# Kernel optimization log

Measured on AMD Instinct MI355X. Metric: run time of the kernel, lower is better.

The kernel has to match this reference:

```python
import jax, jax.numpy as jnp
import numpy as np

BN_EPS = 1e-5
RES_SCALE = 0.7


def setup_inputs() -> dict:
    key = jax.random.key(0)
    ks = jax.random.split(key, 10)
    N, IN_DIM, HID, E, L = 50000, 2000, 64, 1600000, 4
    features = jax.random.normal(ks[0], (N, IN_DIM), dtype=jnp.float32)
    edges = jax.random.randint(ks[1], (2, E), 0, N, dtype=jnp.int64)
    # GCNConv params: layer 0 is in_dim->hid, layers 1..3 are hid->hid
    W0 = jax.random.normal(ks[2], (IN_DIM, HID), dtype=jnp.float32) / np.sqrt(IN_DIM)
    b0 = jnp.zeros((HID,), dtype=jnp.float32)
    Wh = jax.random.normal(ks[3], (L - 1, HID, HID), dtype=jnp.float32) / np.sqrt(HID)
    bh = jnp.zeros((L - 1, HID), dtype=jnp.float32)
    # BatchNorm1d affine params per layer
    gamma = jnp.ones((L, HID), dtype=jnp.float32)
    beta = jnp.zeros((L, HID), dtype=jnp.float32)
    # learned layer-mixing weights (torch.randn init)
    lw = jax.random.normal(ks[4], (L,), dtype=jnp.float32)
    return {"features": features, "edges": edges, "W0": W0, "b0": b0,
            "Wh": Wh, "bh": bh, "gamma": gamma, "beta": beta, "lw": lw}


def reference(features, edges, W0, b0, Wh, bh, gamma, beta, lw):
    n = features.shape[0]
    src, dst = edges[0], edges[1]
    # GCN symmetric normalization with self-loops, edge_weight=1
    deg = jnp.zeros((n,), features.dtype).at[dst].add(1.0) + 1.0  # +1 self loop
    dinv = jax.lax.rsqrt(deg)
    enorm = dinv[src] * dinv[dst]       # [E]
    snorm = dinv * dinv                 # [N], self-loop norm

    def gcn_conv(x, W, b):
        xw = x @ W                                            # [N, H]
        agg = jnp.zeros_like(xw).at[dst].add(xw[src] * enorm[:, None])
        agg = agg + xw * snorm[:, None]
        return agg + b

    def batchnorm(x, g, bt):
        m = x.mean(axis=0)
        v = x.var(axis=0)  # biased variance, as in BN training normalization
        return (x - m) * jax.lax.rsqrt(v + BN_EPS) * g + bt

    L = gamma.shape[0]
    Ws = [W0] + [Wh[i] for i in range(L - 1)]
    bs = [b0] + [bh[i] for i in range(L - 1)]

    layer_out = []
    x = features
    for i in range(L):
        x = gcn_conv(x, Ws[i], bs[i])
        x = jax.nn.relu(batchnorm(x, gamma[i], beta[i]))
        if i > 0:
            x = x + RES_SCALE * layer_out[i - 1]
        layer_out.append(x)

    w = jax.nn.softmax(lw)
    emb = layer_out[0] * w[0]
    for i in range(1, L):
        emb = emb + layer_out[i] * w[i]
    return emb
```

## Files before the change

kernel.cpp:

```cpp
#include <hip/hip_runtime.h>
#include <hip/hip_bf16.h>
#include <math.h>

#define BN_EPS 1e-5f
#define RES_SCALE 0.7f

typedef float f4 __attribute__((ext_vector_type(4)));
typedef short s8 __attribute__((ext_vector_type(8)));

__device__ inline short f2bf(float f) {
    __hip_bfloat16 h = __float2bfloat16(f);
    return *reinterpret_cast<short*>(&h);
}

__global__ __launch_bounds__(256) void k_zero(int* counts, int* cursor, float* stats, int N, int S) {
    int i = blockIdx.x * 256 + threadIdx.x;
    if (i < N) { counts[i] = 0; cursor[i] = 0; }
    if (i < S) stats[i] = 0.0f;
}

__global__ __launch_bounds__(256) void k_count(const int* __restrict__ edges, int E, int* __restrict__ counts) {
    int e = blockIdx.x * 256 + threadIdx.x;
    if (e < E) atomicAdd(&counts[edges[E + e]], 1);
}

__global__ __launch_bounds__(256) void k_scan1(const int* __restrict__ counts, int* __restrict__ bsum,
                                               float* __restrict__ dinv, int N) {
    __shared__ int sd[256];
    int t = threadIdx.x;
    int base = blockIdx.x * 1024 + t * 4;
    int s = 0;
    if (base + 3 < N) {
        int4 v = *(const int4*)(counts + base);
        s = v.x + v.y + v.z + v.w;
        f4 d;
        d.x = rsqrtf((float)v.x + 1.0f);
        d.y = rsqrtf((float)v.y + 1.0f);
        d.z = rsqrtf((float)v.z + 1.0f);
        d.w = rsqrtf((float)v.w + 1.0f);
        *(f4*)(dinv + base) = d;
    } else {
        for (int j = 0; j < 4; ++j) if (base + j < N) {
            int cv = counts[base + j];
            s += cv;
            dinv[base + j] = rsqrtf((float)cv + 1.0f);
        }
    }
    sd[t] = s; __syncthreads();
    for (int off = 128; off > 0; off >>= 1) { if (t < off) sd[t] += sd[t + off]; __syncthreads(); }
    if (t == 0) bsum[blockIdx.x] = sd[0];
}

__global__ void k_scan2(int* bsum, int B, int* rowstart, int N) {
    if (threadIdx.x == 0 && blockIdx.x == 0) {
        int run = 0;
        for (int b = 0; b < B; ++b) { int v = bsum[b]; bsum[b] = run; run += v; }
        rowstart[N] = run;
    }
}

__global__ __launch_bounds__(256) void k_scan3(const int* __restrict__ counts, const int* __restrict__ bsum,
                                               int* __restrict__ rowstart, int N) {
    __shared__ int sd[256];
    int t = threadIdx.x;
    int base = blockIdx.x * 1024 + t * 4;
    int v0 = 0, v1 = 0, v2 = 0, v3 = 0;
    if (base + 3 < N) { int4 v = *(const int4*)(counts + base); v0 = v.x; v1 = v.y; v2 = v.z; v3 = v.w; }
    else {
        if (base < N) v0 = counts[base];
        if (base + 1 < N) v1 = counts[base + 1];
        if (base + 2 < N) v2 = counts[base + 2];
        if (base + 3 < N) v3 = counts[base + 3];
    }
    int s = v0 + v1 + v2 + v3;
    sd[t] = s; __syncthreads();
    for (int off = 1; off < 256; off <<= 1) {
        int add = (t >= off) ? sd[t - off] : 0;
        __syncthreads();
        sd[t] += add;
        __syncthreads();
    }
    int excl = sd[t] - s + bsum[blockIdx.x];
    if (base < N)     rowstart[base]     = excl;
    if (base + 1 < N) rowstart[base + 1] = excl + v0;
    if (base + 2 < N) rowstart[base + 2] = excl + v0 + v1;
    if (base + 3 < N) rowstart[base + 3] = excl + v0 + v1 + v2;
}

__global__ __launch_bounds__(256) void k_scatter(const int* __restrict__ edges, int E,
                                                 const int* __restrict__ rowstart, int* __restrict__ cursor,
                                                 int* __restrict__ colA) {
    int e = blockIdx.x * 256 + threadIdx.x;
    if (e >= E) return;
    int s = edges[e], d = edges[E + e];
    int pos = rowstart[d] + atomicAdd(&cursor[d], 1);
    colA[pos] = s;
}

__global__ __launch_bounds__(256) void k_wt(const float* __restrict__ W0, const float* __restrict__ Wh,
                                            short* __restrict__ WT0, short* __restrict__ WTh, int K0) {
    __shared__ short Ts[64][72];
    int b = blockIdx.x, t = threadIdx.x;
    int nk0 = (K0 + 63) >> 6;
    const float* W; short* dst; int K, kt;
    if (b < nk0) { W = W0; dst = WT0; K = K0; kt = b * 64; }
    else { int l = b - nk0; W = Wh + (size_t)l * 64 * 64; dst = WTh + (size_t)l * 64 * 64; K = 64; kt = 0; }
    #pragma unroll
    for (int i = 0; i < 16; ++i) {
        int idx = t + i * 256;
        int r = idx >> 6, c = idx & 63;
        int gk = kt + r;
        Ts[c][r] = (gk < K) ? f2bf(W[(size_t)gk * 64 + c]) : (short)0;
    }
    __syncthreads();
    #pragma unroll
    for (int i = 0; i < 16; ++i) {
        int idx = t + i * 256;
        int n = idx >> 6, r = idx & 63;
        int gk = kt + r;
        if (gk < K) dst[(size_t)n * K + gk] = Ts[n][r];
    }
}

__global__ __launch_bounds__(256) void k_mm(const float* __restrict__ X, const short* __restrict__ WT,
                                            const float* __restrict__ dinv,
                                            __hip_bfloat16* __restrict__ Cb, int N, int K) {
    __shared__ float Xs[64][68];
    __shared__ short Ws[64][72];
    int t = threadIdx.x;
    int w = t >> 6, lane = t & 63;
    int m = lane & 15, kq = lane >> 4;
    int row0 = blockIdx.x * 64;

    int xr = t >> 3, xc = t & 7;
    int wn = t >> 2, wc = t & 3;

    f4 acc[4] = {};
    f4 px0, px1, px2, px3; int4 pw0, pw1;

    {
        int gr0 = row0 + xr, gr1 = row0 + xr + 32;
        int gk0 = xc * 4, gk1 = 32 + xc * 4;
        px0 = (gr0 < N && gk0 < K) ? *(const f4*)(X + (size_t)gr0 * K + gk0) : (f4){};
        px1 = (gr0 < N && gk1 < K) ? *(const f4*)(X + (size_t)gr0 * K + gk1) : (f4){};
        px2 = (gr1 < N && gk0 < K) ? *(const f4*)(X + (size_t)gr1 * K + gk0) : (f4){};
        px3 = (gr1 < N && gk1 < K) ? *(const f4*)(X + (size_t)gr1 * K + gk1) : (f4){};
        int gw0 = wc * 8, gw1 = 32 + wc * 8;
        pw0 = (gw0 < K) ? *(const int4*)(WT + (size_t)wn * K + gw0) : make_int4(0, 0, 0, 0);
        pw1 = (gw1 < K) ? *(const int4*)(WT + (size_t)wn * K + gw1) : make_int4(0, 0, 0, 0);
    }

    for (int kt = 0; kt < K; kt += 64) {
        *(f4*)&Xs[xr][xc * 4]           = px0;
        *(f4*)&Xs[xr][32 + xc * 4]      = px1;
        *(f4*)&Xs[xr + 32][xc * 4]      = px2;
        *(f4*)&Xs[xr + 32][32 + xc * 4] = px3;
        *(int4*)&Ws[wn][wc * 8]         = pw0;
        *(int4*)&Ws[wn][32 + wc * 8]    = pw1;
        __syncthreads();

        int kn = kt + 64;
        if (kn < K) {
            int gr0 = row0 + xr, gr1 = row0 + xr + 32;
            int gk0 = kn + xc * 4, gk1 = kn + 32 + xc * 4;
            px0 = (gr0 < N && gk0 < K) ? *(const f4*)(X + (size_t)gr0 * K + gk0) : (f4){};
            px1 = (gr0 < N && gk1 < K) ? *(const f4*)(X + (size_t)gr0 * K + gk1) : (f4){};
            px2 = (gr1 < N && gk0 < K) ? *(const f4*)(X + (size_t)gr1 * K + gk0) : (f4){};
            px3 = (gr1 < N && gk1 < K) ? *(const f4*)(X + (size_t)gr1 * K + gk1) : (f4){};
            int gw0 = kn + wc * 8, gw1 = kn + 32 + wc * 8;
            pw0 = (gw0 < K) ? *(const int4*)(WT + (size_t)wn * K + gw0) : make_int4(0, 0, 0, 0);
            pw1 = (gw1 < K) ? *(const int4*)(WT + (size_t)wn * K + gw1) : make_int4(0, 0, 0, 0);
        }

        int arow = w * 16 + m;
        f4 a00 = *(const f4*)&Xs[arow][kq * 8];
        f4 a01 = *(const f4*)&Xs[arow][kq * 8 + 4];
        f4 a10 = *(const f4*)&Xs[arow][32 + kq * 8];
        f4 a11 = *(const f4*)&Xs[arow][32 + kq * 8 + 4];
        s8 av0, av1;
        #pragma unroll
        for (int j = 0; j < 4; ++j) {
            av0[j] = f2bf(a00[j]); av0[j + 4] = f2bf(a01[j]);
            av1[j] = f2bf(a10[j]); av1[j + 4] = f2bf(a11[j]);
        }
        #pragma unroll
        for (int ct = 0; ct < 4; ++ct) {
            s8 bv0 = *(const s8*)&Ws[ct * 16 + m][kq * 8];
            s8 bv1 = *(const s8*)&Ws[ct * 16 + m][32 + kq * 8];
            acc[ct] = __builtin_amdgcn_mfma_f32_16x16x32_bf16(av0, bv0, acc[ct], 0, 0, 0);
            acc[ct] = __builtin_amdgcn_mfma_f32_16x16x32_bf16(av1, bv1, acc[ct], 0, 0, 0);
        }
        __syncthreads();
    }

    #pragma unroll
    for (int reg = 0; reg < 4; ++reg) {
        int gr = row0 + w * 16 + kq * 4 + reg;
        if (gr < N) {
            float di = dinv[gr];
            #pragma unroll
            for (int ct = 0; ct < 4; ++ct)
                Cb[(size_t)gr * 64 + ct * 16 + m] = __float2bfloat16(acc[ct][reg] * di);
        }
    }
}

__device__ inline const unsigned* g_rowsel(const unsigned* xw32, int c, int p, bool lo32) {
    unsigned o0 = (unsigned)__builtin_amdgcn_readlane(c, 2 * p) << 5;
    unsigned o1 = (unsigned)__builtin_amdgcn_readlane(c, 2 * p + 1) << 5;
    return xw32 + (lo32 ? o0 : o1);
}

__global__ __launch_bounds__(256) void k_gather(const __hip_bfloat16* __restrict__ xw, const int* __restrict__ colA,
                                                const int* __restrict__ rowstart,
                                                const float* __restrict__ dinv, float* __restrict__ agg, int N) {
    int wave = (blockIdx.x * 256 + threadIdx.x) >> 6;
    int lane = threadIdx.x & 63;
    if (wave >= N) return;
    int r = wave;
    const unsigned* xw32 = (const unsigned*)xw;
    int l31 = lane & 31;
    bool lo32 = lane < 32;

    unsigned vs = xw32[((size_t)(unsigned)r << 5) | l31];
    float acc0 = lo32 ? __uint_as_float(vs << 16) : 0.0f;
    float acc1 = lo32 ? __uint_as_float(vs & 0xffff0000u) : 0.0f;

    int b = rowstart[r], e = rowstart[r + 1];
    for (int base = b; base < e; base += 64) {
        int idx = base + lane;
        int c = (idx < e) ? colA[idx] : 0;
        int cnt = min(64, e - base);
        int npair = cnt >> 1;
        int j = 0;
        for (; j + 3 < npair; j += 4) {
            unsigned v0 = g_rowsel(xw32, c, j,     lo32)[l31];
            unsigned v1 = g_rowsel(xw32, c, j + 1, lo32)[l31];
            unsigned v2 = g_rowsel(xw32, c, j + 2, lo32)[l31];
            unsigned v3 = g_rowsel(xw32, c, j + 3, lo32)[l31];
            acc0 += __uint_as_float(v0 << 16); acc1 += __uint_as_float(v0 & 0xffff0000u);
            acc0 += __uint_as_float(v1 << 16); acc1 += __uint_as_float(v1 & 0xffff0000u);
            acc0 += __uint_as_float(v2 << 16); acc1 += __uint_as_float(v2 & 0xffff0000u);
            acc0 += __uint_as_float(v3 << 16); acc1 += __uint_as_float(v3 & 0xffff0000u);
        }
        for (; j < npair; ++j) {
            unsigned v = g_rowsel(xw32, c, j, lo32)[l31];
            acc0 += __uint_as_float(v << 16); acc1 += __uint_as_float(v & 0xffff0000u);
        }
        if (cnt & 1) {
            int s = __builtin_amdgcn_readlane(c, cnt - 1);
            unsigned v = xw32[((size_t)(unsigned)s << 5) | l31];
            if (lo32) {
                acc0 += __uint_as_float(v << 16);
                acc1 += __uint_as_float(v & 0xffff0000u);
            }
        }
    }
    acc0 += __shfl_xor(acc0, 32);
    acc1 += __shfl_xor(acc1, 32);
    if (lo32) {
        float di = dinv[r];
        float2 o; o.x = acc0 * di; o.y = acc1 * di;
        *(float2*)(agg + ((size_t)r << 6) + l31 * 2) = o;
    }
}

__global__ __launch_bounds__(256) void k_stats(const float* __restrict__ x, float* __restrict__ stats, int N) {
    int col = threadIdx.x & 63;
    int sub = threadIdx.x >> 6;
    float s = 0.f, s2 = 0.f;
    for (int r = blockIdx.x * 4 + sub; r < N; r += gridDim.x * 4) {
        float v = x[(size_t)r * 64 + col];
        s += v; s2 += v * v;
    }
    __shared__ float sd[2][4][64];
    sd[0][sub][col] = s; sd[1][sub][col] = s2;
    __syncthreads();
    if (sub == 0) {
        s  = sd[0][0][col] + sd[0][1][col] + sd[0][2][col] + sd[0][3][col];
        s2 = sd[1][0][col] + sd[1][1][col] + sd[1][2][col] + sd[1][3][col];
        atomicAdd(&stats[col], s);
        atomicAdd(&stats[64 + col], s2);
    }
}

__global__ __launch_bounds__(256) void k_elem(const float* __restrict__ agg, const float* __restrict__ stats,
                                              const float* __restrict__ gamma, const float* __restrict__ beta,
                                              const float* __restrict__ lw, const float* __restrict__ xprev,
                                              float* __restrict__ xcur, float* __restrict__ emb,
                                              int N, int layer, int L) {
    size_t i = ((size_t)blockIdx.x * 256 + threadIdx.x) * 4;
    if (i >= (size_t)N * 64) return;
    int c = (int)(i & 63);
    float rN = 1.0f / (float)N;
    f4 av = *(const f4*)(agg + i);
    f4 gv = *(const f4*)(gamma + c);
    f4 bv = *(const f4*)(beta + c);
    f4 sv = *(const f4*)(stats + c);
    f4 qv = *(const f4*)(stats + 64 + c);
    f4 v;
    #pragma unroll
    for (int j = 0; j < 4; ++j) {
        float mn = sv[j] * rN;
        float var = qv[j] * rN - mn * mn;
        float inv = rsqrtf(var + BN_EPS);
        v[j] = fmaxf((av[j] - mn) * inv * gv[j] + bv[j], 0.0f);
    }
    f4 xp = {};
    if (layer > 0) {
        xp = *(const f4*)(xprev + i);
        #pragma unroll
        for (int j = 0; j < 4; ++j) v[j] += RES_SCALE * xp[j];
    }
    if (layer < L - 1) *(f4*)(xcur + i) = v;
    if (layer == 0) return;

    float mx = lw[0];
    for (int j = 1; j < L; ++j) mx = fmaxf(mx, lw[j]);
    float sum = 0.f, wbuf[8];
    for (int j = 0; j < L; ++j) { float ee = __expf(lw[j] - mx); wbuf[j] = ee; sum += ee; }
    float rs = 1.0f / sum;
    float wl = wbuf[layer] * rs;
    f4 o;
    if (layer == 1) {
        float w0 = wbuf[0] * rs;
        #pragma unroll
        for (int j = 0; j < 4; ++j) o[j] = w0 * xp[j] + wl * v[j];
    } else {
        f4 ep = *(const f4*)(emb + i);
        #pragma unroll
        for (int j = 0; j < 4; ++j) o[j] = ep[j] + wl * v[j];
    }
    *(f4*)(emb + i) = o;
}

extern "C" void kernel_launch(void* const* d_in, const int* in_sizes, int n_in,
                              void* d_out, int out_size, void* d_ws, size_t ws_size,
                              hipStream_t stream) {
    const float* features = (const float*)d_in[0];
    const int*   edges    = (const int*)d_in[1];
    const float* W0       = (const float*)d_in[2];
    const float* Wh       = (const float*)d_in[4];
    const float* gamma    = (const float*)d_in[6];
    const float* beta     = (const float*)d_in[7];
    const float* lw       = (const float*)d_in[8];

    const int HID    = in_sizes[3];
    const int IN_DIM = in_sizes[2] / HID;
    const int N      = in_sizes[0] / IN_DIM;
    const int E      = in_sizes[1] / 2;
    const int L      = in_sizes[8];
    float* out = (float*)d_out;

    char* ws = (char*)d_ws;
    auto alloc = [&](size_t bytes) { char* p = ws; ws += (bytes + 255) & ~(size_t)255; return p; };
    int*   counts   = (int*)alloc((size_t)N * 4);
    int*   cursor   = (int*)alloc((size_t)N * 4);
    int*   rowstart = (int*)alloc((size_t)(N + 1) * 4);
    int*   bsum     = (int*)alloc(256 * 4);
    float* dinv     = (float*)alloc((size_t)N * 4);
    float* stats    = (float*)alloc((size_t)L * 128 * 4);
    int*   colA     = (int*)alloc((size_t)E * 4);
    short* WT0      = (short*)alloc((size_t)HID * IN_DIM * 2);
    short* WTh      = (short*)alloc((size_t)(L - 1) * HID * HID * 2);
    __hip_bfloat16* xw = (__hip_bfloat16*)alloc((size_t)N * HID * 2);
    float* agg      = (float*)alloc((size_t)N * HID * 4);
    float* x0       = (float*)alloc((size_t)N * HID * 4);
    float* x1       = (float*)alloc((size_t)N * HID * 4);

    int S = L * 128;
    int zgrid = (max(N, S) + 255) / 256;
    k_zero<<<zgrid, 256, 0, stream>>>(counts, cursor, stats, N, S);

    int egrid = (E + 255) / 256;
    k_count<<<egrid, 256, 0, stream>>>(edges, E, counts);

    int B = (N + 1023) / 1024;
    k_scan1<<<B, 256, 0, stream>>>(counts, bsum, dinv, N);
    k_scan2<<<1, 64, 0, stream>>>(bsum, B, rowstart, N);
    k_scan3<<<B, 256, 0, stream>>>(counts, bsum, rowstart, N);
    k_scatter<<<egrid, 256, 0, stream>>>(edges, E, rowstart, cursor, colA);

    int nk0 = (IN_DIM + 63) / 64;
    k_wt<<<nk0 + (L - 1), 256, 0, stream>>>(W0, Wh, WT0, WTh, IN_DIM);

    int mmgrid = (N + 63) / 64;
    int ggrid  = (N + 3) / 4;
    int elgrid = (int)(((size_t)N * HID / 4 + 255) / 256);

    float* xb[2] = { x0, x1 };
    const float* xc_prev = nullptr;
    for (int l = 0; l < L; ++l) {
        const float* Xin = (l == 0) ? features : xc_prev;
        int K = (l == 0) ? IN_DIM : HID;
        const short* WTl = (l == 0) ? WT0 : WTh + (size_t)(l - 1) * HID * HID;
        k_mm<<<mmgrid, 256, 0, stream>>>(Xin, WTl, dinv, xw, N, K);
        k_gather<<<ggrid, 256, 0, stream>>>(xw, colA, rowstart, dinv, agg, N);
        k_stats<<<256, 256, 0, stream>>>(agg, stats + l * 128, N);
        float* xcur = (l < L - 1) ? xb[l & 1] : nullptr;
        const float* xprev = (l == 0) ? nullptr : xb[(l - 1) & 1];
        k_elem<<<elgrid, 256, 0, stream>>>(agg, stats + l * 128, gamma + l * HID, beta + l * HID,
                                           lw, xprev, xcur, out, N, l, L);
        if (l < L - 1) xc_prev = xcur;
    }
}
```

Measured before the change: 1.006 ms.

## Fuse BN/residual elementwise with next-layer 64x64 matmul; double-buffer prefetch in k_mm

```diff
diff --git a/kernel.cpp b/kernel.cpp
--- a/kernel.cpp
+++ b/kernel.cpp
@@ -7,6 +7,7 @@
 
 typedef float f4 __attribute__((ext_vector_type(4)));
 typedef short s8 __attribute__((ext_vector_type(8)));
+typedef short bs4 __attribute__((ext_vector_type(4)));
 
 __device__ inline short f2bf(float f) {
     __hip_bfloat16 h = __float2bfloat16(f);
@@ -122,6 +123,50 @@
     }
 }
 
+#define MM_ISSUE(PX0, PX1, PX2, PX3, PW0, PW1, KT)                                        \
+    {                                                                                      \
+        int gr0_ = row0 + xr, gr1_ = gr0_ + 32;                                            \
+        int gk0_ = (KT) + xc * 4, gk1_ = (KT) + 32 + xc * 4;                               \
+        PX0 = (gr0_ < N && gk0_ < K) ? *(const f4*)(X + (size_t)gr0_ * K + gk0_) : (f4){}; \
+        PX1 = (gr0_ < N && gk1_ < K) ? *(const f4*)(X + (size_t)gr0_ * K + gk1_) : (f4){}; \
+        PX2 = (gr1_ < N && gk0_ < K) ? *(const f4*)(X + (size_t)gr1_ * K + gk0_) : (f4){}; \
+        PX3 = (gr1_ < N && gk1_ < K) ? *(const f4*)(X + (size_t)gr1_ * K + gk1_) : (f4){}; \
+        int gw0_ = (KT) + wc * 8, gw1_ = (KT) + 32 + wc * 8;                               \
+        PW0 = (gw0_ < K) ? *(const int4*)(WT + (size_t)wn * K + gw0_) : make_int4(0,0,0,0);\
+        PW1 = (gw1_ < K) ? *(const int4*)(WT + (size_t)wn * K + gw1_) : make_int4(0,0,0,0);\
+    }
+
+#define MM_BODY(PX0, PX1, PX2, PX3, PW0, PW1, KT)                                          \
+    {                                                                                      \
+        *(f4*)&Xs[xr][xc * 4]           = PX0;                                             \
+        *(f4*)&Xs[xr][32 + xc * 4]      = PX1;                                             \
+        *(f4*)&Xs[xr + 32][xc * 4]      = PX2;                                             \
+        *(f4*)&Xs[xr + 32][32 + xc * 4] = PX3;                                             \
+        *(int4*)&Ws[wn][wc * 8]         = PW0;                                             \
+        *(int4*)&Ws[wn][32 + wc * 8]    = PW1;                                             \
+        if ((KT) + 128 < K) MM_ISSUE(PX0, PX1, PX2, PX3, PW0, PW1, (KT) + 128);            \
+        __syncthreads();                                                                   \
+        int arow_ = w * 16 + m;                                                            \
+        f4 a00 = *(const f4*)&Xs[arow_][kq * 8];                                           \
+        f4 a01 = *(const f4*)&Xs[arow_][kq * 8 + 4];                                       \
+        f4 a10 = *(const f4*)&Xs[arow_][32 + kq * 8];                                      \
+        f4 a11 = *(const f4*)&Xs[arow_][32 + kq * 8 + 4];                                  \
+        s8 av0, av1;                                                                       \
+        _Pragma("unroll")                                                                  \
+        for (int j = 0; j < 4; ++j) {                                                      \
+            av0[j] = f2bf(a00[j]); av0[j + 4] = f2bf(a01[j]);                              \
+            av1[j] = f2bf(a10[j]); av1[j + 4] = f2bf(a11[j]);                              \
+        }                                                                                  \
+        _Pragma("unroll")                                                                  \
+        for (int ct = 0; ct < 4; ++ct) {                                                   \
+            s8 bv0 = *(const s8*)&Ws[ct * 16 + m][kq * 8];                                 \
+            s8 bv1 = *(const s8*)&Ws[ct * 16 + m][32 + kq * 8];                            \
+            acc[ct] = __builtin_amdgcn_mfma_f32_16x16x32_bf16(av0, bv0, acc[ct], 0, 0, 0); \
+            acc[ct] = __builtin_amdgcn_mfma_f32_16x16x32_bf16(av1, bv1, acc[ct], 0, 0, 0); \
+        }                                                                                  \
+        __syncthreads();                                                                   \
+    }
+
 __global__ __launch_bounds__(256) void k_mm(const float* __restrict__ X, const short* __restrict__ WT,
                                             const float* __restrict__ dinv,
                                             __hip_bfloat16* __restrict__ Cb, int N, int K) {
@@ -136,61 +181,15 @@
     int wn = t >> 2, wc = t & 3;
 
     f4 acc[4] = {};
-    f4 px0, px1, px2, px3; int4 pw0, pw1;
-
-    {
-        int gr0 = row0 + xr, gr1 = row0 + xr + 32;
-        int gk0 = xc * 4, gk1 = 32 + xc * 4;
-        px0 = (gr0 < N && gk0 < K) ? *(const f4*)(X + (size_t)gr0 * K + gk0) : (f4){};
-        px1 = (gr0 < N && gk1 < K) ? *(const f4*)(X + (size_t)gr0 * K + gk1) : (f4){};
-        px2 = (gr1 < N && gk0 < K) ? *(const f4*)(X + (size_t)gr1 * K + gk0) : (f4){};
-        px3 = (gr1 < N && gk1 < K) ? *(const f4*)(X + (size_t)gr1 * K + gk1) : (f4){};
-        int gw0 = wc * 8, gw1 = 32 + wc * 8;
-        pw0 = (gw0 < K) ? *(const int4*)(WT + (size_t)wn * K + gw0) : make_int4(0, 0, 0, 0);
-        pw1 = (gw1 < K) ? *(const int4*)(WT + (size_t)wn * K + gw1) : make_int4(0, 0, 0, 0);
-    }
-
-    for (int kt = 0; kt < K; kt += 64) {
-        *(f4*)&Xs[xr][xc * 4]           = px0;
-        *(f4*)&Xs[xr][32 + xc * 4]      = px1;
-        *(f4*)&Xs[xr + 32][xc * 4]      = px2;
-        *(f4*)&Xs[xr + 32][32 + xc * 4] = px3;
-        *(int4*)&Ws[wn][wc * 8]         = pw0;
-        *(int4*)&Ws[wn][32 + wc * 8]    = pw1;
-        __syncthreads();
-
-        int kn = kt + 64;
-        if (kn < K) {
-            int gr0 = row0 + xr, gr1 = row0 + xr + 32;
-            int gk0 = kn + xc * 4, gk1 = kn + 32 + xc * 4;
-            px0 = (gr0 < N && gk0 < K) ? *(const f4*)(X + (size_t)gr0 * K + gk0) : (f4){};
-            px1 = (gr0 < N && gk1 < K) ? *(const f4*)(X + (size_t)gr0 * K + gk1) : (f4){};
-            px2 = (gr1 < N && gk0 < K) ? *(const f4*)(X + (size_t)gr1 * K + gk0) : (f4){};
-            px3 = (gr1 < N && gk1 < K) ? *(const f4*)(X + (size_t)gr1 * K + gk1) : (f4){};
-            int gw0 = kn + wc * 8, gw1 = kn + 32 + wc * 8;
-            pw0 = (gw0 < K) ? *(const int4*)(WT + (size_t)wn * K + gw0) : make_int4(0, 0, 0, 0);
-            pw1 = (gw1 < K) ? *(const int4*)(WT + (size_t)wn * K + gw1) : make_int4(0, 0, 0, 0);
-        }
-
-        int arow = w * 16 + m;
-        f4 a00 = *(const f4*)&Xs[arow][kq * 8];
-        f4 a01 = *(const f4*)&Xs[arow][kq * 8 + 4];
-        f4 a10 = *(const f4*)&Xs[arow][32 + kq * 8];
-        f4 a11 = *(const f4*)&Xs[arow][32 + kq * 8 + 4];
-        s8 av0, av1;
-        #pragma unroll
-        for (int j = 0; j < 4; ++j) {
-            av0[j] = f2bf(a00[j]); av0[j + 4] = f2bf(a01[j]);
-            av1[j] = f2bf(a10[j]); av1[j + 4] = f2bf(a11[j]);
-        }
-        #pragma unroll
-        for (int ct = 0; ct < 4; ++ct) {
-            s8 bv0 = *(const s8*)&Ws[ct * 16 + m][kq * 8];
-            s8 bv1 = *(const s8*)&Ws[ct * 16 + m][32 + kq * 8];
-            acc[ct] = __builtin_amdgcn_mfma_f32_16x16x32_bf16(av0, bv0, acc[ct], 0, 0, 0);
-            acc[ct] = __builtin_amdgcn_mfma_f32_16x16x32_bf16(av1, bv1, acc[ct], 0, 0, 0);
-        }
-        __syncthreads();
+    f4 pxA0, pxA1, pxA2, pxA3; int4 pwA0, pwA1;
+    f4 pxB0, pxB1, pxB2, pxB3; int4 pwB0, pwB1;
+
+    MM_ISSUE(pxA0, pxA1, pxA2, pxA3, pwA0, pwA1, 0);
+    if (64 < K) MM_ISSUE(pxB0, pxB1, pxB2, pxB3, pwB0, pwB1, 64);
+
+    for (int kt = 0; kt < K; kt += 128) {
+        MM_BODY(pxA0, pxA1, pxA2, pxA3, pwA0, pwA1, kt);
+        if (kt + 64 < K) MM_BODY(pxB0, pxB1, pxB2, pxB3, pwB0, pwB1, kt + 64);
     }
 
     #pragma unroll
@@ -284,6 +283,105 @@
     }
 }
 
+__global__ __launch_bounds__(256) void k_elemmm(const float* __restrict__ agg, const float* __restrict__ stats,
+                                                const float* __restrict__ gamma, const float* __restrict__ beta,
+                                                const float* __restrict__ lw, const float* __restrict__ xprev,
+                                                float* __restrict__ xcur, float* __restrict__ emb,
+                                                const short* __restrict__ WT, const float* __restrict__ dinv,
+                                                __hip_bfloat16* __restrict__ xw,
+                                                int N, int layer, int L) {
+    __shared__ short Xb[64][72];
+    __shared__ short Ws[64][72];
+    int t = threadIdx.x;
+    int row0 = blockIdx.x * 64;
+
+    {
+        int n = t >> 3, c8 = (t & 7) * 8;
+        *(int4*)&Ws[n][c8]      = *(const int4*)(WT + n * 64 + c8);
+        *(int4*)&Ws[n + 32][c8] = *(const int4*)(WT + (n + 32) * 64 + c8);
+    }
+
+    int r = t >> 2, q = t & 3;
+    int gr = row0 + r;
+    bool valid = gr < N;
+    float rN = 1.0f / (float)N;
+    size_t base = (size_t)gr * 64 + q * 16;
+
+    float mx = lw[0];
+    for (int j = 1; j < L; ++j) mx = fmaxf(mx, lw[j]);
+    float sum = 0.f, wbuf[8];
+    for (int j = 0; j < L; ++j) { float ee = __expf(lw[j] - mx); wbuf[j] = ee; sum += ee; }
+    float rs = 1.0f / sum;
+    float wl = wbuf[layer] * rs, w0 = wbuf[0] * rs;
+
+    #pragma unroll
+    for (int j = 0; j < 4; ++j) {
+        int c = q * 16 + j * 4;
+        f4 av = valid ? *(const f4*)(agg + base + j * 4) : (f4){};
+        f4 sv = *(const f4*)(stats + c);
+        f4 qv = *(const f4*)(stats + 64 + c);
+        f4 gv = *(const f4*)(gamma + c);
+        f4 bv = *(const f4*)(beta + c);
+        f4 v;
+        #pragma unroll
+        for (int jj = 0; jj < 4; ++jj) {
+            float mn = sv[jj] * rN;
+            float var = qv[jj] * rN - mn * mn;
+            float inv = rsqrtf(var + BN_EPS);
+            v[jj] = fmaxf((av[jj] - mn) * inv * gv[jj] + bv[jj], 0.0f);
+        }
+        f4 xp = {};
+        if (layer > 0) {
+            if (valid) xp = *(const f4*)(xprev + base + j * 4);
+            #pragma unroll
+            for (int jj = 0; jj < 4; ++jj) v[jj] += RES_SCALE * xp[jj];
+        }
+        if (valid) *(f4*)(xcur + base + j * 4) = v;
+        if (layer >= 1 && valid) {
+            f4 o;
+            if (layer == 1) {
+                #pragma unroll
+                for (int jj = 0; jj < 4; ++jj) o[jj] = w0 * xp[jj] + wl * v[jj];
+            } else {
+                f4 ep = *(const f4*)(emb + base + j * 4);
+                #pragma unroll
+                for (int jj = 0; jj < 4; ++jj) o[jj] = ep[jj] + wl * v[jj];
+            }
+            *(f4*)(emb + base + j * 4) = o;
+        }
+        bs4 xb;
+        #pragma unroll
+        for (int jj = 0; jj < 4; ++jj) xb[jj] = f2bf(v[jj]);
+        *(bs4*)&Xb[r][q * 16 + j * 4] = xb;
+    }
+    __syncthreads();
+
+    int w = t >> 6, lane = t & 63;
+    int m = lane & 15, kq = lane >> 4;
+    f4 acc[4] = {};
+    int arow = w * 16 + m;
+    s8 av0 = *(const s8*)&Xb[arow][kq * 8];
+    s8 av1 = *(const s8*)&Xb[arow][32 + kq * 8];
+    #pragma unroll
+    for (int ct = 0; ct < 4; ++ct) {
+        s8 bv0 = *(const s8*)&Ws[ct * 16 + m][kq * 8];
+        s8 bv1 = *(const s8*)&Ws[ct * 16 + m][32 + kq * 8];
+        acc[ct] = __builtin_amdgcn_mfma_f32_16x16x32_bf16(av0, bv0, acc[ct], 0, 0, 0);
+        acc[ct] = __builtin_amdgcn_mfma_f32_16x16x32_bf16(av1, bv1, acc[ct], 0, 0, 0);
+    }
+
+    #pragma unroll
+    for (int reg = 0; reg < 4; ++reg) {
+        int gro = row0 + w * 16 + kq * 4 + reg;
+        if (gro < N) {
+            float di = dinv[gro];
+            #pragma unroll
+            for (int ct = 0; ct < 4; ++ct)
+                xw[(size_t)gro * 64 + ct * 16 + m] = __float2bfloat16(acc[ct][reg] * di);
+        }
+    }
+}
+
 __global__ __launch_bounds__(256) void k_elem(const float* __restrict__ agg, const float* __restrict__ stats,
                                               const float* __restrict__ gamma, const float* __restrict__ beta,
                                               const float* __restrict__ lw, const float* __restrict__ xprev,
@@ -388,19 +486,22 @@
     int ggrid  = (N + 3) / 4;
     int elgrid = (int)(((size_t)N * HID / 4 + 255) / 256);
 
+    k_mm<<<mmgrid, 256, 0, stream>>>(features, WT0, dinv, xw, N, IN_DIM);
+
     float* xb[2] = { x0, x1 };
-    const float* xc_prev = nullptr;
     for (int l = 0; l < L; ++l) {
-        const float* Xin = (l == 0) ? features : xc_prev;
-        int K = (l == 0) ? IN_DIM : HID;
-        const short* WTl = (l == 0) ? WT0 : WTh + (size_t)(l - 1) * HID * HID;
-        k_mm<<<mmgrid, 256, 0, stream>>>(Xin, WTl, dinv, xw, N, K);
         k_gather<<<ggrid, 256, 0, stream>>>(xw, colA, rowstart, dinv, agg, N);
         k_stats<<<256, 256, 0, stream>>>(agg, stats + l * 128, N);
-        float* xcur = (l < L - 1) ? xb[l & 1] : nullptr;
-        const float* xprev = (l == 0) ? nullptr : xb[(l - 1) & 1];
-        k_elem<<<elgrid, 256, 0, stream>>>(agg, stats + l * 128, gamma + l * HID, beta + l * HID,
-                                           lw, xprev, xcur, out, N, l, L);
-        if (l < L - 1) xc_prev = xcur;
-    }
-}
+        if (l < L - 1) {
+            float* xcur = xb[l & 1];
+            const float* xprev = (l == 0) ? nullptr : xb[(l - 1) & 1];
+            k_elemmm<<<mmgrid, 256, 0, stream>>>(agg, stats + l * 128, gamma + l * HID, beta + l * HID,
+                                                 lw, xprev, xcur, out,
+                                                 WTh + (size_t)l * HID * HID, dinv, xw, N, l, L);
+        } else {
+            const float* xprev = xb[(l - 1) & 1];
+            k_elem<<<elgrid, 256, 0, stream>>>(agg, stats + l * 128, gamma + l * HID, beta + l * HID,
+                                               lw, xprev, nullptr, out, N, l, L);
+        }
+    }
+}
```

Result: slower. 1.035 ms (+2.9%).
